# Optimization experiments

Hardware: AMD Instinct MI355X
Metric: run time of the kernel (lower is better)

## Reference

```python
import jax, jax.numpy as jnp
import numpy as np

B, T, D, H, DFF = 2, 2048, 1024, 16, 4096
K = D // H  # head size = 64
EPS = 1e-5


def _layernorm(x, g, b):
    mu = jnp.mean(x, axis=-1, keepdims=True)
    var = jnp.mean(jnp.square(x - mu), axis=-1, keepdims=True)
    return (x - mu) * jax.lax.rsqrt(var + EPS) * g + b


def setup_inputs() -> dict:
    key = jax.random.key(0)
    ks = jax.random.split(key, 12)
    s_attn = 1.0 / np.sqrt(D)
    s_ff1 = 1.0 / np.sqrt(D)
    s_ff2 = 1.0 / np.sqrt(DFF)
    return {
        "x": jax.random.normal(ks[0], (B, T, D), jnp.float32),
        # per-head q/k/v projections, stacked: [H, D, K] (each head's Linear has no bias)
        "Wq": jax.random.normal(ks[1], (H, D, K), jnp.float32) * s_attn,
        "Wk": jax.random.normal(ks[2], (H, D, K), jnp.float32) * s_attn,
        "Wv": jax.random.normal(ks[3], (H, D, K), jnp.float32) * s_attn,
        "Wo": jax.random.normal(ks[4], (D, D), jnp.float32) * s_attn,
        "bo": jax.random.normal(ks[5], (D,), jnp.float32) * 0.01,
        "W1": jax.random.normal(ks[6], (D, DFF), jnp.float32) * s_ff1,
        "b1": jax.random.normal(ks[7], (DFF,), jnp.float32) * 0.01,
        "W2": jax.random.normal(ks[8], (DFF, D), jnp.float32) * s_ff2,
        "b2": jax.random.normal(ks[9], (D,), jnp.float32) * 0.01,
        "g1": jnp.ones((D,), jnp.float32),
        "be1": jnp.zeros((D,), jnp.float32),
        "g2": jnp.ones((D,), jnp.float32),
        "be2": jnp.zeros((D,), jnp.float32),
    }


def reference(x, Wq, Wk, Wv, Wo, bo, W1, b1, W2, b2, g1, be1, g2, be2):
    b, t, d = x.shape
    h = _layernorm(x, g1, be1)
    # multi-head attention (per-head linear projections, fused via einsum)
    q = jnp.einsum('btd,hdk->bhtk', h, Wq)
    k = jnp.einsum('btd,hdk->bhtk', h, Wk)
    v = jnp.einsum('btd,hdk->bhtk', h, Wv)
    scores = jnp.einsum('bhtk,bhsk->bhts', q, k) * (K ** -0.5)
    causal = jnp.tril(jnp.ones((t, t), bool))
    scores = jnp.where(causal, scores, -jnp.inf)
    attn = jax.nn.softmax(scores, axis=-1)
    o = jnp.einsum('bhts,bhsk->bhtk', attn, v)
    o = o.transpose(0, 2, 1, 3).reshape(b, t, d)  # concat heads
    x = x + o @ Wo + bo
    # feed-forward (exact GELU, as torch default)
    h2 = _layernorm(x, g2, be2)
    ff = jax.nn.gelu(h2 @ W1 + b1, approximate=False) @ W2 + b2
    return x + ff
```

## Files before the change

kernel.cpp:

```cpp
#include <hip/hip_runtime.h>
#include <hip/hip_bf16.h>


#define BT   4096
#define DIM  1024
#define DFF  4096
#define TSEQ 2048
#define NHEAD 16
#define HDIM 64
#define QKV_LD 3072

typedef __attribute__((ext_vector_type(8))) short  bf16x8;
typedef __attribute__((ext_vector_type(4))) float  floatx4;

__device__ __forceinline__ void async_copy16(const __hip_bfloat16* g, __hip_bfloat16* l) {
    __builtin_amdgcn_global_load_lds(
        (const __attribute__((address_space(1))) void*)g,
        (__attribute__((address_space(3))) void*)l, 16, 0, 0);
}

__device__ __forceinline__ floatx4 mfma_bf16(bf16x8 a, bf16x8 b, floatx4 c) {
    return __builtin_amdgcn_mfma_f32_16x16x32_bf16(a, b, c, 0, 0, 0);
}

__global__ __launch_bounds__(256) void ln_kernel(const float* __restrict__ x,
                                                 const float* __restrict__ g,
                                                 const float* __restrict__ be,
                                                 __hip_bfloat16* __restrict__ out) {
    const int row = blockIdx.x;
    const int t = threadIdx.x;
    const float4 v = ((const float4*)(x + (size_t)row * DIM))[t];
    float s  = v.x + v.y + v.z + v.w;
    float ss = v.x * v.x + v.y * v.y + v.z * v.z + v.w * v.w;
    for (int d = 1; d < 64; d <<= 1) { s += __shfl_xor(s, d); ss += __shfl_xor(ss, d); }
    __shared__ float red[8];
    const int w = t >> 6;
    if ((t & 63) == 0) { red[w] = s; red[w + 4] = ss; }
    __syncthreads();
    s  = red[0] + red[1] + red[2] + red[3];
    ss = red[4] + red[5] + red[6] + red[7];
    const float mu = s * (1.0f / DIM);
    const float rstd = rsqrtf(ss * (1.0f / DIM) - mu * mu + 1e-5f);
    const float4 gv = ((const float4*)g)[t];
    const float4 bv = ((const float4*)be)[t];
    __hip_bfloat16* o = out + (size_t)row * DIM + t * 4;
    o[0] = __float2bfloat16((v.x - mu) * rstd * gv.x + bv.x);
    o[1] = __float2bfloat16((v.y - mu) * rstd * gv.y + bv.y);
    o[2] = __float2bfloat16((v.z - mu) * rstd * gv.z + bv.z);
    o[3] = __float2bfloat16((v.w - mu) * rstd * gv.w + bv.w);
}

__global__ __launch_bounds__(256) void transpose_cast(const float* __restrict__ src, int src_ld,
                                                      __hip_bfloat16* __restrict__ dst, int dst_ld) {
    __shared__ float tile[64][65];
    const int r0 = blockIdx.x * 64, c0 = blockIdx.y * 64;
    const int tr = threadIdx.x >> 6;
    const int tc = threadIdx.x & 63;
    for (int i = 0; i < 16; ++i) {
        const int r = i * 4 + tr;
        tile[r][tc] = src[(size_t)(r0 + r) * src_ld + c0 + tc];
    }
    __syncthreads();
    for (int i = 0; i < 16; ++i) {
        const int c = i * 4 + tr;
        dst[(size_t)(c0 + c) * dst_ld + r0 + tc] = __float2bfloat16(tile[tc][c]);
    }
}

__global__ __launch_bounds__(256) void transpose_qkv(const float* __restrict__ Wq,
                                                     const float* __restrict__ Wk,
                                                     const float* __restrict__ Wv,
                                                     __hip_bfloat16* __restrict__ dst) {
    __shared__ float tile[64][65];
    const int hz = blockIdx.y;
    const int proj = hz >> 4, h = hz & 15;
    const float* W = (proj == 0 ? Wq : (proj == 1 ? Wk : Wv)) + (size_t)h * DIM * HDIM;
    const int r0 = blockIdx.x * 64;
    const int tr = threadIdx.x >> 6;
    const int tc = threadIdx.x & 63;
    for (int i = 0; i < 16; ++i) {
        const int r = i * 4 + tr;
        tile[r][tc] = W[(size_t)(r0 + r) * HDIM + tc];
    }
    __syncthreads();
    for (int i = 0; i < 16; ++i) {
        const int k = i * 4 + tr;
        dst[(size_t)(proj * 1024 + h * 64 + k) * DIM + r0 + tc] = __float2bfloat16(tile[tc][k]);
    }
}

__global__ __launch_bounds__(256) void transpose_v(const __hip_bfloat16* __restrict__ qkv,
                                                   __hip_bfloat16* __restrict__ vt) {
    __shared__ __align__(16) __hip_bfloat16 tile[64 * 72];
    const int t = threadIdx.x;
    const int bh = blockIdx.y;
    const int b = bh >> 4, h = bh & 15;
    const int t0 = blockIdx.x * 64;
    const __hip_bfloat16* src = qkv + (size_t)b * TSEQ * QKV_LD + 2048 + h * HDIM;
    const int lo = t >> 3, k8 = t & 7;
    for (int i = 0; i < 2; ++i) {
        const int rr = i * 32 + lo;
        const bf16x8 v = *(const bf16x8*)(src + (size_t)(t0 + rr) * QKV_LD + k8 * 8);
        const int cb = k8 ^ ((rr >> 3) & 7);
        *(bf16x8*)(tile + rr * 72 + cb * 8) = v;
    }
    __syncthreads();
    for (int i = 0; i < 2; ++i) {
        const int dd = i * 32 + lo;
        const int c0 = dd >> 3, cl = dd & 7;
        bf16x8 o;
        for (int jj = 0; jj < 8; ++jj) {
            const int key = k8 * 8 + jj;
            o[jj] = *(const short*)(tile + key * 72 + (c0 ^ ((key >> 3) & 7)) * 8 + cl);
        }
        *(bf16x8*)(vt + ((size_t)bh * HDIM + dd) * TSEQ + t0 + k8 * 8) = o;
    }
}

template <int EPI>
__global__ __launch_bounds__(256) void gemm_bt(const __hip_bfloat16* __restrict__ A,
                                               const __hip_bfloat16* __restrict__ Bt,
                                               __hip_bfloat16* __restrict__ outb,
                                               const float* __restrict__ bias,
                                               int M, int N, int K) {
    __shared__ __align__(16) __hip_bfloat16 As[2][128 * 32];
    __shared__ __align__(16) __hip_bfloat16 Bs[2][128 * 32];
    const int t = threadIdx.x;
    const int w = t >> 6, l = t & 63;
    const int quad = l >> 4, tl = l & 15;
    const int wr = w >> 1, wc = w & 1;
    const int m0 = blockIdx.y * 128, n0 = blockIdx.x * 128;

    floatx4 acc[4][4] = {};
    const int rowA = t >> 2;
    const int c8 = (t & 3) << 3;

    for (int k0 = 0; k0 < K; k0 += 64) {
        __syncthreads();
        for (int half = 0; half < 2; ++half) {
            const int kk = k0 + half * 32;
            const __hip_bfloat16* gA = A + (size_t)(m0 + rowA) * K + kk + c8;
            const __hip_bfloat16* gB = Bt + (size_t)(n0 + rowA) * K + kk + c8;
            async_copy16(gA,                  As[half] + w * 512);
            async_copy16(gA + (size_t)64 * K, As[half] + 2048 + w * 512);
            async_copy16(gB,                  Bs[half] + w * 512);
            async_copy16(gB + (size_t)64 * K, Bs[half] + 2048 + w * 512);
        }
        __syncthreads();

        for (int ks = 0; ks < 2; ++ks) {
            bf16x8 af[4], bfr[4];
            const int aRow = wr * 64 + tl;
            const int bRow = wc * 64 + tl;
            for (int mi = 0; mi < 4; ++mi)
                af[mi] = *(const bf16x8*)(As[ks] + (aRow + mi * 16) * 32 + quad * 8);
            for (int ni = 0; ni < 4; ++ni)
                bfr[ni] = *(const bf16x8*)(Bs[ks] + (bRow + ni * 16) * 32 + quad * 8);
            for (int mi = 0; mi < 4; ++mi)
                for (int ni = 0; ni < 4; ++ni)
                    acc[mi][ni] = mfma_bf16(af[mi], bfr[ni], acc[mi][ni]);
        }
    }

    const int rowBase = m0 + wr * 64 + quad * 4;
    const int colBase = n0 + wc * 64 + tl;
    for (int mi = 0; mi < 4; ++mi) {
        for (int ni = 0; ni < 4; ++ni) {
            const int c = colBase + ni * 16;
            for (int j = 0; j < 4; ++j) {
                const int r = rowBase + mi * 16 + j;
                const size_t idx = (size_t)r * N + c;
                float v = acc[mi][ni][j];
                if (EPI == 1) {
                    v += bias[c];
                    v = 0.5f * v * (1.0f + erff(v * 0.70710678118654752f));
                }
                outb[idx] = __float2bfloat16(v);
            }
        }
    }
}

__global__ __launch_bounds__(256) void gemm_bt_k64(const __hip_bfloat16* __restrict__ A,
                                                   const __hip_bfloat16* __restrict__ Bt,
                                                   float* __restrict__ outf,
                                                   const float* __restrict__ bias,
                                                   const float* __restrict__ resid,
                                                   int M, int N, int K) {
    __shared__ __align__(16) __hip_bfloat16 As[128 * 64];
    __shared__ __align__(16) __hip_bfloat16 Bs[64 * 64];
    const int t = threadIdx.x;
    const int w = t >> 6, l = t & 63;
    const int quad = l >> 4, tl = l & 15;
    const int id = blockIdx.x;
    const int xcd = id & 7, jb = id >> 3;
    const int n0 = (jb & 15) * 64;
    const int m0 = ((jb >> 4) * 8 + xcd) * 128;

    floatx4 acc[2][4] = {};
    const int srow = t >> 3;
    const int scg  = t & 7;

    for (int k0 = 0; k0 < K; k0 += 64) {
        __syncthreads();
        for (int i = 0; i < 4; ++i) {
            const int row = i * 32 + srow;
            async_copy16(A + (size_t)(m0 + row) * K + k0 + ((scg ^ (row & 7)) << 3),
                         As + i * 2048 + w * 512);
        }
        for (int i = 0; i < 2; ++i) {
            const int row = i * 32 + srow;
            async_copy16(Bt + (size_t)(n0 + row) * K + k0 + ((scg ^ (row & 7)) << 3),
                         Bs + i * 2048 + w * 512);
        }
        __syncthreads();

        for (int ks = 0; ks < 2; ++ks) {
            bf16x8 af[2], bfr[4];
            for (int mi = 0; mi < 2; ++mi) {
                const int r = w * 32 + mi * 16 + tl;
                af[mi] = *(const bf16x8*)(As + r * 64 + (((ks * 4 + quad) ^ (r & 7)) << 3));
            }
            for (int ni = 0; ni < 4; ++ni) {
                const int r = ni * 16 + tl;
                bfr[ni] = *(const bf16x8*)(Bs + r * 64 + (((ks * 4 + quad) ^ (r & 7)) << 3));
            }
            for (int mi = 0; mi < 2; ++mi)
                for (int ni = 0; ni < 4; ++ni)
                    acc[mi][ni] = mfma_bf16(af[mi], bfr[ni], acc[mi][ni]);
        }
    }

    const int rowBase = m0 + w * 32 + quad * 4;
    const int colBase = n0 + tl;
    for (int mi = 0; mi < 2; ++mi) {
        for (int ni = 0; ni < 4; ++ni) {
            const int c = colBase + ni * 16;
            for (int j = 0; j < 4; ++j) {
                const int r = rowBase + mi * 16 + j;
                const size_t idx = (size_t)r * N + c;
                outf[idx] = resid[idx] + acc[mi][ni][j] + bias[c];
            }
        }
    }
}

#define KS_LD 72
#define VT_LD 72
#define PL_LD 72
__global__ __launch_bounds__(256) void attn_kernel(const __hip_bfloat16* __restrict__ qkv,
                                                   const __hip_bfloat16* __restrict__ vt,
                                                   __hip_bfloat16* __restrict__ out) {
    __shared__ __align__(16) __hip_bfloat16 Ks[64 * KS_LD];
    __shared__ __align__(16) __hip_bfloat16 Vts[64 * VT_LD];
    __shared__ __align__(16) __hip_bfloat16 Pl[4][16 * PL_LD];
    const int t = threadIdx.x;
    const int w = t >> 6, l = t & 63;
    const int quad = l >> 4, tl = l & 15;
    const int id = blockIdx.x;
    const int bh = ((id & 7) << 2) | ((id >> 3) & 3);
    const int pq = id >> 5;
    const int b = bh >> 4, h = bh & 15;
    const __hip_bfloat16* Qp  = qkv + (size_t)b * TSEQ * QKV_LD + h * HDIM;
    const __hip_bfloat16* Kp  = Qp + 1024;
    const __hip_bfloat16* Vtp = vt + (size_t)bh * HDIM * TSEQ;
    __hip_bfloat16* P = Pl[w];
    const float cscale = 0.125f * 1.4426950408889634f;
    const int srow = t >> 3, sk8 = t & 7;

    for (int half = 0; half < 2; ++half) {
        const int qb = half ? (31 - pq) : pq;
        const int qw = qb * 64 + w * 16;
        const int nb = qb + 1;

        const __hip_bfloat16* qrow = Qp + (size_t)(qw + tl) * QKV_LD + quad * 8;
        const bf16x8 qf0 = *(const bf16x8*)qrow;
        const bf16x8 qf1 = *(const bf16x8*)(qrow + 32);
        floatx4 oacc[4] = {};
        float l_i[4] = {0.0f, 0.0f, 0.0f, 0.0f};
        const int myrow = quad * 4;

        for (int it = 0; it < nb; ++it) {
            const int s0 = it * 64;
            __syncthreads();
            for (int i = 0; i < 2; ++i) {
                const int rr = i * 32 + srow;
                const bf16x8 kv = *(const bf16x8*)(Kp  + (size_t)(s0 + rr) * QKV_LD + sk8 * 8);
                const bf16x8 vv = *(const bf16x8*)(Vtp + (size_t)rr * TSEQ + s0 + sk8 * 8);
                *(bf16x8*)(Ks  + rr * KS_LD + sk8 * 8) = kv;
                *(bf16x8*)(Vts + rr * VT_LD + sk8 * 8) = vv;
            }
            __syncthreads();

            floatx4 sc[4];
            for (int ni = 0; ni < 4; ++ni) {
                const __hip_bfloat16* kr = Ks + (ni * 16 + tl) * KS_LD + quad * 8;
                floatx4 z = {0.0f, 0.0f, 0.0f, 0.0f};
                z = mfma_bf16(qf0, *(const bf16x8*)kr, z);
                sc[ni] = mfma_bf16(qf1, *(const bf16x8*)(kr + 32), z);
            }

            const bool lastB = (it == nb - 1);
            for (int ni = 0; ni < 4; ++ni) {
                const int keyrel = ni * 16 + tl - w * 16;
                for (int j = 0; j < 4; ++j) {
                    float pv = exp2f(sc[ni][j] * cscale);
                    if (lastB && keyrel > myrow + j) pv = 0.0f;
                    l_i[j] += pv;
                    P[(myrow + j) * PL_LD + ni * 16 + tl] = __float2bfloat16(pv);
                }
            }
            __builtin_amdgcn_wave_barrier();

            for (int kc = 0; kc < 2; ++kc) {
                const bf16x8 pf = *(const bf16x8*)(P + tl * PL_LD + kc * 32 + quad * 8);
                for (int ni = 0; ni < 4; ++ni) {
                    const bf16x8 vf = *(const bf16x8*)(Vts + (ni * 16 + tl) * VT_LD
                                                       + kc * 32 + quad * 8);
                    oacc[ni] = mfma_bf16(pf, vf, oacc[ni]);
                }
            }
        }

        for (int d = 1; d < 16; d <<= 1) {
            float r0 = __shfl_xor(l_i[0], d), r1 = __shfl_xor(l_i[1], d);
            float r2 = __shfl_xor(l_i[2], d), r3 = __shfl_xor(l_i[3], d);
            l_i[0] += r0; l_i[1] += r1; l_i[2] += r2; l_i[3] += r3;
        }
        for (int j = 0; j < 4; ++j) {
            const float inv = 1.0f / l_i[j];
            const int rg = qw + quad * 4 + j;
            __hip_bfloat16* orow = out + ((size_t)b * TSEQ + rg) * DIM + h * HDIM;
            for (int ni = 0; ni < 4; ++ni)
                orow[ni * 16 + tl] = __float2bfloat16(oacc[ni][j] * inv);
        }
    }
}

extern "C" void kernel_launch(void* const* d_in, const int* in_sizes, int n_in,
                              void* d_out, int out_size, void* d_ws, size_t ws_size,
                              hipStream_t stream) {
    const float* x   = (const float*)d_in[0];
    const float* Wq  = (const float*)d_in[1];
    const float* Wk  = (const float*)d_in[2];
    const float* Wv  = (const float*)d_in[3];
    const float* Wo  = (const float*)d_in[4];
    const float* bo  = (const float*)d_in[5];
    const float* W1  = (const float*)d_in[6];
    const float* b1  = (const float*)d_in[7];
    const float* W2  = (const float*)d_in[8];
    const float* b2  = (const float*)d_in[9];
    const float* g1  = (const float*)d_in[10];
    const float* be1 = (const float*)d_in[11];
    const float* g2  = (const float*)d_in[12];
    const float* be2 = (const float*)d_in[13];
    float* out = (float*)d_out;

    size_t off = 0;
    char* wsb = (char*)d_ws;
    auto carve = [&](size_t bytes) {
        void* p = wsb + off;
        off += (bytes + 255) & ~(size_t)255;
        return p;
    };
    __hip_bfloat16* WqkvT = (__hip_bfloat16*)carve((size_t)3072 * 1024 * 2);
    __hip_bfloat16* WoT   = (__hip_bfloat16*)carve((size_t)1024 * 1024 * 2);
    __hip_bfloat16* W1T   = (__hip_bfloat16*)carve((size_t)4096 * 1024 * 2);
    __hip_bfloat16* W2T   = (__hip_bfloat16*)carve((size_t)1024 * 4096 * 2);
    __hip_bfloat16* h1    = (__hip_bfloat16*)carve((size_t)BT * DIM * 2);
    __hip_bfloat16* qkv   = (__hip_bfloat16*)carve((size_t)BT * QKV_LD * 2);
    __hip_bfloat16* vtb   = (__hip_bfloat16*)carve((size_t)BT * DIM * 2);
    __hip_bfloat16* att   = (__hip_bfloat16*)carve((size_t)BT * DIM * 2);
    float*          x2    = (float*)carve((size_t)BT * DIM * 4);
    __hip_bfloat16* h2    = (__hip_bfloat16*)carve((size_t)BT * DIM * 2);
    __hip_bfloat16* ff1   = (__hip_bfloat16*)carve((size_t)BT * DFF * 2);

    transpose_qkv<<<dim3(16, 48), 256, 0, stream>>>(Wq, Wk, Wv, WqkvT);
    transpose_cast<<<dim3(16, 16), 256, 0, stream>>>(Wo, 1024, WoT, 1024);
    transpose_cast<<<dim3(16, 64), 256, 0, stream>>>(W1, 4096, W1T, 1024);
    transpose_cast<<<dim3(64, 16), 256, 0, stream>>>(W2, 1024, W2T, 4096);

    ln_kernel<<<BT, 256, 0, stream>>>(x, g1, be1, h1);
    gemm_bt<0><<<dim3(24, 32), 256, 0, stream>>>(h1, WqkvT, qkv, nullptr, BT, QKV_LD, DIM);
    transpose_v<<<dim3(32, 32), 256, 0, stream>>>(qkv, vtb);
    attn_kernel<<<512, 256, 0, stream>>>(qkv, vtb, att);
    gemm_bt_k64<<<512, 256, 0, stream>>>(att, WoT, x2, bo, x, BT, DIM, DIM);
    ln_kernel<<<BT, 256, 0, stream>>>(x2, g2, be2, h2);
    gemm_bt<1><<<dim3(32, 32), 256, 0, stream>>>(h2, W1T, ff1, b1, BT, DFF, DIM);
    gemm_bt_k64<<<512, 256, 0, stream>>>(ff1, W2T, out, b2, x2, BT, DIM, DFF);
}
```

Measured before the change: 372.0 us.

## Merge weight transposes and first layernorm into one prep launch; deepen K tile to 128

```diff
diff --git a/kernel.cpp b/kernel.cpp
--- a/kernel.cpp
+++ b/kernel.cpp
@@ -23,17 +23,16 @@
     return __builtin_amdgcn_mfma_f32_16x16x32_bf16(a, b, c, 0, 0, 0);
 }
 
-__global__ __launch_bounds__(256) void ln_kernel(const float* __restrict__ x,
-                                                 const float* __restrict__ g,
-                                                 const float* __restrict__ be,
-                                                 __hip_bfloat16* __restrict__ out) {
-    const int row = blockIdx.x;
+__device__ __forceinline__ void ln_body(const float* __restrict__ x,
+                                        const float* __restrict__ g,
+                                        const float* __restrict__ be,
+                                        __hip_bfloat16* __restrict__ out,
+                                        int row, float* red) {
     const int t = threadIdx.x;
     const float4 v = ((const float4*)(x + (size_t)row * DIM))[t];
     float s  = v.x + v.y + v.z + v.w;
     float ss = v.x * v.x + v.y * v.y + v.z * v.z + v.w * v.w;
     for (int d = 1; d < 64; d <<= 1) { s += __shfl_xor(s, d); ss += __shfl_xor(ss, d); }
-    __shared__ float red[8];
     const int w = t >> 6;
     if ((t & 63) == 0) { red[w] = s; red[w + 4] = ss; }
     __syncthreads();
@@ -50,42 +49,75 @@
     o[3] = __float2bfloat16((v.w - mu) * rstd * gv.w + bv.w);
 }
 
-__global__ __launch_bounds__(256) void transpose_cast(const float* __restrict__ src, int src_ld,
-                                                      __hip_bfloat16* __restrict__ dst, int dst_ld) {
-    __shared__ float tile[64][65];
-    const int r0 = blockIdx.x * 64, c0 = blockIdx.y * 64;
+__global__ __launch_bounds__(256) void ln_kernel(const float* __restrict__ x,
+                                                 const float* __restrict__ g,
+                                                 const float* __restrict__ be,
+                                                 __hip_bfloat16* __restrict__ out) {
+    __shared__ float red[8];
+    ln_body(x, g, be, out, blockIdx.x, red);
+}
+
+__device__ __forceinline__ void tc_body(const float* __restrict__ src, int src_ld,
+                                        __hip_bfloat16* __restrict__ dst, int dst_ld,
+                                        int bx, int by, float* tile ) {
+    const int r0 = bx * 64, c0 = by * 64;
     const int tr = threadIdx.x >> 6;
     const int tc = threadIdx.x & 63;
     for (int i = 0; i < 16; ++i) {
         const int r = i * 4 + tr;
-        tile[r][tc] = src[(size_t)(r0 + r) * src_ld + c0 + tc];
+        tile[r * 65 + tc] = src[(size_t)(r0 + r) * src_ld + c0 + tc];
     }
     __syncthreads();
     for (int i = 0; i < 16; ++i) {
         const int c = i * 4 + tr;
-        dst[(size_t)(c0 + c) * dst_ld + r0 + tc] = __float2bfloat16(tile[tc][c]);
-    }
-}
-
-__global__ __launch_bounds__(256) void transpose_qkv(const float* __restrict__ Wq,
-                                                     const float* __restrict__ Wk,
-                                                     const float* __restrict__ Wv,
-                                                     __hip_bfloat16* __restrict__ dst) {
-    __shared__ float tile[64][65];
-    const int hz = blockIdx.y;
-    const int proj = hz >> 4, h = hz & 15;
-    const float* W = (proj == 0 ? Wq : (proj == 1 ? Wk : Wv)) + (size_t)h * DIM * HDIM;
-    const int r0 = blockIdx.x * 64;
-    const int tr = threadIdx.x >> 6;
-    const int tc = threadIdx.x & 63;
-    for (int i = 0; i < 16; ++i) {
-        const int r = i * 4 + tr;
-        tile[r][tc] = W[(size_t)(r0 + r) * HDIM + tc];
-    }
-    __syncthreads();
-    for (int i = 0; i < 16; ++i) {
-        const int k = i * 4 + tr;
-        dst[(size_t)(proj * 1024 + h * 64 + k) * DIM + r0 + tc] = __float2bfloat16(tile[tc][k]);
+        dst[(size_t)(c0 + c) * dst_ld + r0 + tc] = __float2bfloat16(tile[tc * 65 + c]);
+    }
+}
+
+__global__ __launch_bounds__(256) void prep_kernel(const float* __restrict__ x,
+                                                   const float* __restrict__ g1,
+                                                   const float* __restrict__ be1,
+                                                   const float* __restrict__ Wq,
+                                                   const float* __restrict__ Wk,
+                                                   const float* __restrict__ Wv,
+                                                   const float* __restrict__ Wo,
+                                                   const float* __restrict__ W1,
+                                                   const float* __restrict__ W2,
+                                                   __hip_bfloat16* __restrict__ h1,
+                                                   __hip_bfloat16* __restrict__ WqkvT,
+                                                   __hip_bfloat16* __restrict__ WoT,
+                                                   __hip_bfloat16* __restrict__ W1T,
+                                                   __hip_bfloat16* __restrict__ W2T) {
+    __shared__ __align__(16) float smemf[64 * 65];
+    const int id = blockIdx.x;
+    if (id < 4096) {
+        ln_body(x, g1, be1, h1, id, smemf);
+    } else if (id < 4096 + 768) {
+        const int i = id - 4096;
+        const int bx = i & 15, hz = i >> 4;
+        const int proj = hz >> 4, h = hz & 15;
+        const float* W = (proj == 0 ? Wq : (proj == 1 ? Wk : Wv)) + (size_t)h * DIM * HDIM;
+        const int r0 = bx * 64;
+        const int tr = threadIdx.x >> 6, tc = threadIdx.x & 63;
+        for (int i2 = 0; i2 < 16; ++i2) {
+            const int r = i2 * 4 + tr;
+            smemf[r * 65 + tc] = W[(size_t)(r0 + r) * HDIM + tc];
+        }
+        __syncthreads();
+        for (int i2 = 0; i2 < 16; ++i2) {
+            const int k = i2 * 4 + tr;
+            WqkvT[(size_t)(proj * 1024 + h * 64 + k) * DIM + r0 + tc] =
+                __float2bfloat16(smemf[tc * 65 + k]);
+        }
+    } else if (id < 4096 + 768 + 256) {
+        const int i = id - (4096 + 768);
+        tc_body(Wo, 1024, WoT, 1024, i & 15, i >> 4, smemf);
+    } else if (id < 4096 + 768 + 256 + 1024) {
+        const int i = id - (4096 + 768 + 256);
+        tc_body(W1, 4096, W1T, 1024, i & 15, i >> 4, smemf);
+    } else {
+        const int i = id - (4096 + 768 + 256 + 1024);
+        tc_body(W2, 1024, W2T, 4096, i & 63, i >> 6, smemf);
     }
 }
 
@@ -181,14 +213,14 @@
     }
 }
 
-__global__ __launch_bounds__(256) void gemm_bt_k64(const __hip_bfloat16* __restrict__ A,
-                                                   const __hip_bfloat16* __restrict__ Bt,
-                                                   float* __restrict__ outf,
-                                                   const float* __restrict__ bias,
-                                                   const float* __restrict__ resid,
-                                                   int M, int N, int K) {
-    __shared__ __align__(16) __hip_bfloat16 As[128 * 64];
-    __shared__ __align__(16) __hip_bfloat16 Bs[64 * 64];
+__global__ __launch_bounds__(256) void gemm_bt_k128(const __hip_bfloat16* __restrict__ A,
+                                                    const __hip_bfloat16* __restrict__ Bt,
+                                                    float* __restrict__ outf,
+                                                    const float* __restrict__ bias,
+                                                    const float* __restrict__ resid,
+                                                    int M, int N, int K) {
+    __shared__ __align__(16) __hip_bfloat16 As[128 * 128];
+    __shared__ __align__(16) __hip_bfloat16 Bs[64 * 128];
     const int t = threadIdx.x;
     const int w = t >> 6, l = t & 63;
     const int quad = l >> 4, tl = l & 15;
@@ -198,32 +230,32 @@
     const int m0 = ((jb >> 4) * 8 + xcd) * 128;
 
     floatx4 acc[2][4] = {};
-    const int srow = t >> 3;
-    const int scg  = t & 7;
-
-    for (int k0 = 0; k0 < K; k0 += 64) {
+    const int srow = t >> 4;
+    const int scg  = t & 15;
+
+    for (int k0 = 0; k0 < K; k0 += 128) {
         __syncthreads();
-        for (int i = 0; i < 4; ++i) {
-            const int row = i * 32 + srow;
+        for (int p = 0; p < 8; ++p) {
+            const int row = p * 16 + srow;
             async_copy16(A + (size_t)(m0 + row) * K + k0 + ((scg ^ (row & 7)) << 3),
-                         As + i * 2048 + w * 512);
-        }
-        for (int i = 0; i < 2; ++i) {
-            const int row = i * 32 + srow;
+                         As + p * 2048 + w * 512);
+        }
+        for (int p = 0; p < 4; ++p) {
+            const int row = p * 16 + srow;
             async_copy16(Bt + (size_t)(n0 + row) * K + k0 + ((scg ^ (row & 7)) << 3),
-                         Bs + i * 2048 + w * 512);
+                         Bs + p * 2048 + w * 512);
         }
         __syncthreads();
 
-        for (int ks = 0; ks < 2; ++ks) {
+        for (int ks = 0; ks < 4; ++ks) {
             bf16x8 af[2], bfr[4];
             for (int mi = 0; mi < 2; ++mi) {
                 const int r = w * 32 + mi * 16 + tl;
-                af[mi] = *(const bf16x8*)(As + r * 64 + (((ks * 4 + quad) ^ (r & 7)) << 3));
+                af[mi] = *(const bf16x8*)(As + r * 128 + (((ks * 4 + quad) ^ (r & 7)) << 3));
             }
             for (int ni = 0; ni < 4; ++ni) {
                 const int r = ni * 16 + tl;
-                bfr[ni] = *(const bf16x8*)(Bs + r * 64 + (((ks * 4 + quad) ^ (r & 7)) << 3));
+                bfr[ni] = *(const bf16x8*)(Bs + r * 128 + (((ks * 4 + quad) ^ (r & 7)) << 3));
             }
             for (int mi = 0; mi < 2; ++mi)
                 for (int ni = 0; ni < 4; ++ni)
@@ -375,17 +407,13 @@
     __hip_bfloat16* h2    = (__hip_bfloat16*)carve((size_t)BT * DIM * 2);
     __hip_bfloat16* ff1   = (__hip_bfloat16*)carve((size_t)BT * DFF * 2);
 
-    transpose_qkv<<<dim3(16, 48), 256, 0, stream>>>(Wq, Wk, Wv, WqkvT);
-    transpose_cast<<<dim3(16, 16), 256, 0, stream>>>(Wo, 1024, WoT, 1024);
-    transpose_cast<<<dim3(16, 64), 256, 0, stream>>>(W1, 4096, W1T, 1024);
-    transpose_cast<<<dim3(64, 16), 256, 0, stream>>>(W2, 1024, W2T, 4096);
-
-    ln_kernel<<<BT, 256, 0, stream>>>(x, g1, be1, h1);
+    prep_kernel<<<7168, 256, 0, stream>>>(x, g1, be1, Wq, Wk, Wv, Wo, W1, W2,
+                                          h1, WqkvT, WoT, W1T, W2T);
     gemm_bt<0><<<dim3(24, 32), 256, 0, stream>>>(h1, WqkvT, qkv, nullptr, BT, QKV_LD, DIM);
     transpose_v<<<dim3(32, 32), 256, 0, stream>>>(qkv, vtb);
     attn_kernel<<<512, 256, 0, stream>>>(qkv, vtb, att);
-    gemm_bt_k64<<<512, 256, 0, stream>>>(att, WoT, x2, bo, x, BT, DIM, DIM);
+    gemm_bt_k128<<<512, 256, 0, stream>>>(att, WoT, x2, bo, x, BT, DIM, DIM);
     ln_kernel<<<BT, 256, 0, stream>>>(x2, g2, be2, h2);
     gemm_bt<1><<<dim3(32, 32), 256, 0, stream>>>(h2, W1T, ff1, b1, BT, DFF, DIM);
-    gemm_bt_k64<<<512, 256, 0, stream>>>(ff1, W2T, out, b2, x2, BT, DIM, DFF);
-}
+    gemm_bt_k128<<<512, 256, 0, stream>>>(ff1, W2T, out, b2, x2, BT, DIM, DFF);
+}
```

Measured after the change: 356.2 us. 4.2% less time.
